# Kernel tuning notes

Measured on AMD Instinct MI355X. Metric: run time of the kernel, lower is better.

Reference implementation:

```python
import jax, jax.numpy as jnp
import numpy as np

N = 100000   # nodes
E = 1600000  # edges
NF = 8       # node features
H = 128      # hid_channel


def _gcn(x, ei, W, b):
    """PyG GCNConv: add self-loops, sym-normalize, x@W then scatter-add, +bias."""
    n = x.shape[0]
    loop = jnp.arange(n)
    s = jnp.concatenate([ei[0], loop])
    d = jnp.concatenate([ei[1], loop])
    deg = jax.ops.segment_sum(jnp.ones_like(s, jnp.float32), d, num_segments=n)
    dinv = jnp.where(deg > 0, jax.lax.rsqrt(deg), 0.0)
    norm = dinv[s] * dinv[d]                       # [E+n]
    xw = x @ W                                     # [n, out]
    out = jax.ops.segment_sum(xw[s] * norm[:, None], d, num_segments=n)
    return out + b


def _dag_pool(x, ei, k):
    """DAGPool(k): contiguous-k mean clustering; unpool restores saved (x, ei)."""
    n = x.shape[0]
    nc = -(-n // k)
    cid = jnp.arange(n) // k
    cnt = jax.ops.segment_sum(jnp.ones((n,), jnp.float32), cid, num_segments=nc)
    xp = jax.ops.segment_sum(x, cid, num_segments=nc) / cnt[:, None]
    return xp, ei // k, (x, ei)


def setup_inputs() -> dict:
    key = jax.random.key(0)
    ks = jax.random.split(key, 24)

    def w(k, i, o):
        return jax.random.normal(k, (i, o), jnp.float32) / np.sqrt(i).astype(np.float32)

    d = {
        "x": jax.random.normal(ks[0], (N, NF), jnp.float32),
        "edge_index": jax.random.randint(ks[1], (E, 2), 0, N, dtype=jnp.int64),
        "c1W": w(ks[2], NF, H),          "c1b": jnp.zeros((H,), jnp.float32),
        "c2W": w(ks[3], H + NF, H),      "c2b": jnp.zeros((H,), jnp.float32),
        "c3W": w(ks[4], H + NF, H),      "c3b": jnp.zeros((H,), jnp.float32),
        "c4W": w(ks[5], H, H),           "c4b": jnp.zeros((H,), jnp.float32),
        "c5W": w(ks[6], H, H),           "c5b": jnp.zeros((H,), jnp.float32),
        "f1W": w(ks[7], 2 * H + NF, H),  "f1b": jnp.zeros((H,), jnp.float32),
        "f2W": w(ks[8], 2 * H, H),       "f2b": jnp.zeros((H,), jnp.float32),
        "f3W": w(ks[9], 2 * H, H),       "f3b": jnp.zeros((H,), jnp.float32),
        "f4W": w(ks[10], H + NF, H),     "f4b": jnp.zeros((H,), jnp.float32),
        "f5W": w(ks[11], H + NF, 1),     "f5b": jnp.zeros((1,), jnp.float32),
    }
    return d


def reference(x, edge_index, c1W, c1b, c2W, c2b, c3W, c3b, c4W, c4b, c5W, c5b,
              f1W, f1b, f2W, f2b, f3W, f3b, f4W, f4b, f5W, f5b):
    ei = edge_index.T  # [2, E]
    x_in = x
    h = jax.nn.relu(_gcn(x, ei, c1W, c1b))
    h = jnp.concatenate([h, x_in], axis=-1)
    h = jax.nn.relu(_gcn(h, ei, c2W, c2b))
    h = jnp.concatenate([x_in, h], axis=-1)            # [N, NF+H]

    xp1, ei1, un1 = _dag_pool(h, ei, 5)
    t = jax.nn.relu(_gcn(xp1, ei1, c3W, c3b))
    t = jax.nn.relu(jnp.concatenate([xp1, t], -1) @ f1W + f1b)
    xp2, ei2, un2 = _dag_pool(t, ei1, 3)
    t = jax.nn.relu(_gcn(xp2, ei2, c4W, c4b))
    t = jax.nn.relu(jnp.concatenate([xp2, t], -1) @ f2W + f2b)
    xp3, ei3, un3 = _dag_pool(t, ei2, 3)
    t = jax.nn.relu(_gcn(xp3, ei3, c5W, c5b))
    t = jax.nn.relu(jnp.concatenate([xp3, t], -1) @ f3W + f3b)
    # unpool chain discards pooled features and restores pre-pool1 state
    xr, _ = un1

    h = jax.nn.relu(xr @ f4W + f4b)
    out = jax.nn.sigmoid(jnp.concatenate([x_in, h], -1) @ f5W + f5b)
    return out.ravel()  # [N], binary (num_classes==2 -> 1 logit)
```

## Files before the change

kernel.cpp:

```cpp
#include <hip/hip_runtime.h>
#include <hip/hip_bf16.h>
#include <math.h>


#define NBUK 128

typedef __attribute__((ext_vector_type(8))) short short8;
typedef __attribute__((ext_vector_type(4))) float f32x4;

__device__ __forceinline__ unsigned short f32_to_bf16_rne(float f) {
    unsigned u = __float_as_uint(f);
    return (unsigned short)((u + 0x7fffu + ((u >> 16) & 1u)) >> 16);
}

__global__ __launch_bounds__(512) void bucket_kernel(
    const int* __restrict__ ei, int* __restrict__ bcnt_pad,
    int2* __restrict__ bucket, int E, int N, int cap) {
    constexpr int EPB = 8192;
    __shared__ int lcnt[NBUK];
    __shared__ int lcur[NBUK];
    int e0 = blockIdx.x * EPB;
    int e1 = min(e0 + EPB, E);
    if (threadIdx.x < NBUK) lcnt[threadIdx.x] = 0;
    __syncthreads();
    for (int e = e0 + threadIdx.x; e < e1; e += 512) {
        int2 v = ((const int2*)ei)[e];
        if ((unsigned)v.y < (unsigned)N) {
            int b = (int)(((unsigned long long)(unsigned)v.y * NBUK) / (unsigned)N);
            atomicAdd(&lcnt[b], 1);
        }
    }
    __syncthreads();
    if (threadIdx.x < NBUK)
        lcur[threadIdx.x] = atomicAdd(&bcnt_pad[threadIdx.x * 16], lcnt[threadIdx.x]);
    __syncthreads();
    for (int e = e0 + threadIdx.x; e < e1; e += 512) {
        int2 v = ((const int2*)ei)[e];
        if ((unsigned)v.y < (unsigned)N) {
            int b = (int)(((unsigned long long)(unsigned)v.y * NBUK) / (unsigned)N);
            int pos = atomicAdd(&lcur[b], 1);
            if (pos < cap) {
                int s = ((unsigned)v.x < (unsigned)N) ? v.x : 0;
                bucket[(size_t)b * cap + pos] = make_int2(s, v.y);
            }
        }
    }
}

__global__ __launch_bounds__(1024) void csr_kernel(
    const int2* __restrict__ bucket, const int* __restrict__ bcnt_pad,
    int* __restrict__ cnt, int* __restrict__ rowstart, int* __restrict__ col,
    int N, int cap) {
    __shared__ int lcnt[1024];
    __shared__ int lscan[1024];
    int b = blockIdx.x;
    int lo = (int)(((long long)b * N + NBUK - 1) / NBUK);
    int hi = (int)(((long long)(b + 1) * N + NBUK - 1) / NBUK);
    int range = hi - lo;
    lcnt[threadIdx.x] = 0;
    __syncthreads();
    int n = min(bcnt_pad[b * 16], cap);
    const int2* bk = bucket + (size_t)b * cap;
    for (int i = threadIdx.x; i < n; i += 1024)
        atomicAdd(&lcnt[bk[i].y - lo], 1);
    __syncthreads();
    int myc = lcnt[threadIdx.x];
    if ((int)threadIdx.x < range) cnt[lo + threadIdx.x] = myc;
    lscan[threadIdx.x] = myc;
    __syncthreads();
    for (int off = 1; off < 1024; off <<= 1) {
        int y = (threadIdx.x >= off) ? lscan[threadIdx.x - off] : 0;
        __syncthreads();
        lscan[threadIdx.x] += y;
        __syncthreads();
    }
    int colbase = b * cap;
    int excl = lscan[threadIdx.x] - myc;
    if ((int)threadIdx.x < range) rowstart[lo + threadIdx.x] = colbase + excl;
    lcnt[threadIdx.x] = excl;
    __syncthreads();
    for (int i = threadIdx.x; i < n; i += 1024) {
        int2 v = bk[i];
        int pos = atomicAdd(&lcnt[v.y - lo], 1);
        col[(size_t)colbase + pos] = v.x;
    }
}

__global__ __launch_bounds__(256) void dinv_xs_kernel(const int* __restrict__ cnt,
                                                      const float* __restrict__ x,
                                                      float* __restrict__ dinv,
                                                      float* __restrict__ xs,
                                                      unsigned short* __restrict__ Abf2,
                                                      int n) {
    int v = blockIdx.x * 256 + threadIdx.x;
    if (v >= n) return;
    float dv = rsqrtf((float)(cnt[v] + 1));
    dinv[v] = dv;
    const float4* x4 = (const float4*)x;
    float4 a = x4[v * 2], b = x4[v * 2 + 1];
    float4* o = (float4*)xs;
    o[v * 2]     = make_float4(a.x * dv, a.y * dv, a.z * dv, a.w * dv);
    o[v * 2 + 1] = make_float4(b.x * dv, b.y * dv, b.z * dv, b.w * dv);
    unsigned short u[8] = {f32_to_bf16_rne(a.x), f32_to_bf16_rne(a.y),
                           f32_to_bf16_rne(a.z), f32_to_bf16_rne(a.w),
                           f32_to_bf16_rne(b.x), f32_to_bf16_rne(b.y),
                           f32_to_bf16_rne(b.z), f32_to_bf16_rne(b.w)};
    ulonglong2 pk;
    pk.x = (unsigned long long)u[0] | ((unsigned long long)u[1] << 16)
         | ((unsigned long long)u[2] << 32) | ((unsigned long long)u[3] << 48);
    pk.y = (unsigned long long)u[4] | ((unsigned long long)u[5] << 16)
         | ((unsigned long long)u[6] << 32) | ((unsigned long long)u[7] << 48);
    *(ulonglong2*)&Abf2[(size_t)v * 160] = pk;
    ulonglong2 z; z.x = 0ull; z.y = 0ull;
    *(ulonglong2*)&Abf2[(size_t)v * 160 + 136] = z;
    *(ulonglong2*)&Abf2[(size_t)v * 160 + 144] = z;
    *(ulonglong2*)&Abf2[(size_t)v * 160 + 152] = z;
}

__global__ __launch_bounds__(256) void agg8_kernel(const float* __restrict__ xs,
                                                   const int* __restrict__ rowstart,
                                                   const int* __restrict__ cnt,
                                                   const int* __restrict__ col,
                                                   const float* __restrict__ dinv,
                                                   float* __restrict__ aggx,
                                                   unsigned short* __restrict__ Abf,
                                                   int n) {
    int v = blockIdx.x * 256 + threadIdx.x;
    if (v >= n) return;
    const float4* r4 = (const float4*)xs;
    float4 a = make_float4(0, 0, 0, 0), b = make_float4(0, 0, 0, 0);
    int start = rowstart[v];
    int end = start + cnt[v];
    for (int j = start; j < end; j++) {
        int s = col[j];
        float4 p = r4[(size_t)s * 2], q = r4[(size_t)s * 2 + 1];
        a.x += p.x; a.y += p.y; a.z += p.z; a.w += p.w;
        b.x += q.x; b.y += q.y; b.z += q.z; b.w += q.w;
    }
    float4 p = r4[(size_t)v * 2], q = r4[(size_t)v * 2 + 1];
    a.x += p.x; a.y += p.y; a.z += p.z; a.w += p.w;
    b.x += q.x; b.y += q.y; b.z += q.z; b.w += q.w;
    float dv = dinv[v];
    a = make_float4(a.x * dv, a.y * dv, a.z * dv, a.w * dv);
    b = make_float4(b.x * dv, b.y * dv, b.z * dv, b.w * dv);
    float4* o = (float4*)aggx;
    o[(size_t)v * 2]     = a;
    o[(size_t)v * 2 + 1] = b;
    unsigned short u[8] = {f32_to_bf16_rne(a.x), f32_to_bf16_rne(a.y),
                           f32_to_bf16_rne(a.z), f32_to_bf16_rne(a.w),
                           f32_to_bf16_rne(b.x), f32_to_bf16_rne(b.y),
                           f32_to_bf16_rne(b.z), f32_to_bf16_rne(b.w)};
    ulonglong2 pk;
    pk.x = (unsigned long long)u[0] | ((unsigned long long)u[1] << 16)
         | ((unsigned long long)u[2] << 32) | ((unsigned long long)u[3] << 48);
    pk.y = (unsigned long long)u[4] | ((unsigned long long)u[5] << 16)
         | ((unsigned long long)u[6] << 32) | ((unsigned long long)u[7] << 48);
    *(ulonglong2*)&Abf[(size_t)v * 160 + 128] = pk;
    ulonglong2 z; z.x = 0ull; z.y = 0ull;
    *(ulonglong2*)&Abf[(size_t)v * 160 + 136] = z;
    *(ulonglong2*)&Abf[(size_t)v * 160 + 144] = z;
    *(ulonglong2*)&Abf[(size_t)v * 160 + 152] = z;
}

__global__ __launch_bounds__(256) void agg128_kernel(const unsigned* __restrict__ rows,
                                                     const int* __restrict__ rowstart,
                                                     const int* __restrict__ cnt,
                                                     const int* __restrict__ col,
                                                     const float* __restrict__ dinv,
                                                     unsigned short* __restrict__ Abf,
                                                     int n) {
    int v = blockIdx.x * 4 + (threadIdx.x >> 6);
    int lane = threadIdx.x & 63;
    if (v >= n) return;
    float ax = 0.f, ay = 0.f;
    int start = rowstart[v];
    int end = start + cnt[v];
    for (int base = start; base < end; base += 64) {
        int m = end - base; if (m > 64) m = 64;
        int si = (lane < m) ? col[base + lane] : 0;
        int t = 0;
        for (; t + 4 <= m; t += 4) {
            int s0 = __shfl(si, t),     s1 = __shfl(si, t + 1);
            int s2 = __shfl(si, t + 2), s3 = __shfl(si, t + 3);
            unsigned u0 = rows[(size_t)s0 * 64 + lane];
            unsigned u1 = rows[(size_t)s1 * 64 + lane];
            unsigned u2 = rows[(size_t)s2 * 64 + lane];
            unsigned u3 = rows[(size_t)s3 * 64 + lane];
            ax += (__uint_as_float(u0 << 16) + __uint_as_float(u1 << 16))
                + (__uint_as_float(u2 << 16) + __uint_as_float(u3 << 16));
            ay += (__uint_as_float(u0 & 0xffff0000u) + __uint_as_float(u1 & 0xffff0000u))
                + (__uint_as_float(u2 & 0xffff0000u) + __uint_as_float(u3 & 0xffff0000u));
        }
        for (; t < m; t++) {
            int s = __shfl(si, t);
            unsigned u = rows[(size_t)s * 64 + lane];
            ax += __uint_as_float(u << 16);
            ay += __uint_as_float(u & 0xffff0000u);
        }
    }
    unsigned us = rows[(size_t)v * 64 + lane];
    ax += __uint_as_float(us << 16);
    ay += __uint_as_float(us & 0xffff0000u);
    float dv = dinv[v];
    unsigned pk = (unsigned)f32_to_bf16_rne(ax * dv)
                | ((unsigned)f32_to_bf16_rne(ay * dv) << 16);
    ((unsigned*)Abf)[(size_t)v * 80 + lane] = pk;
}

__global__ __launch_bounds__(256) void gemm8_kernel(
    const float* __restrict__ A1, const float* __restrict__ W,
    const float* __restrict__ bias, const float* __restrict__ dinv,
    unsigned short* __restrict__ out, int n) {
    constexpr int K = 8, KP = 12, NPB = 32;
    __shared__ float lds[NPB * KP];
    int node0 = blockIdx.x * NPB;
    for (int idx = threadIdx.x; idx < NPB * K; idx += 256) {
        int r = idx / K, k = idx - r * K;
        int node = node0 + r;
        lds[r * KP + k] = (node < n) ? A1[(size_t)node * K + k] : 0.f;
    }
    __syncthreads();
    int f8 = threadIdx.x & 15, ng = threadIdx.x >> 4;
    int fbase = f8 * 8;
    float acc[2][8];
#pragma unroll
    for (int r = 0; r < 2; r++)
#pragma unroll
        for (int j = 0; j < 8; j++) acc[r][j] = 0.f;
    for (int k = 0; k < K; k += 4) {
        float4 wlo[4], whi[4];
#pragma unroll
        for (int kk = 0; kk < 4; kk++) {
            wlo[kk] = *(const float4*)&W[(size_t)(k + kk) * 128 + fbase];
            whi[kk] = *(const float4*)&W[(size_t)(k + kk) * 128 + fbase + 4];
        }
#pragma unroll
        for (int r = 0; r < 2; r++) {
            float4 a = *(const float4*)&lds[(2 * ng + r) * KP + k];
            float av[4] = {a.x, a.y, a.z, a.w};
#pragma unroll
            for (int kk = 0; kk < 4; kk++) {
                acc[r][0] += av[kk] * wlo[kk].x; acc[r][1] += av[kk] * wlo[kk].y;
                acc[r][2] += av[kk] * wlo[kk].z; acc[r][3] += av[kk] * wlo[kk].w;
                acc[r][4] += av[kk] * whi[kk].x; acc[r][5] += av[kk] * whi[kk].y;
                acc[r][6] += av[kk] * whi[kk].z; acc[r][7] += av[kk] * whi[kk].w;
            }
        }
    }
    float4 blo = *(const float4*)&bias[fbase];
    float4 bhi = *(const float4*)&bias[fbase + 4];
    float bv[8] = {blo.x, blo.y, blo.z, blo.w, bhi.x, bhi.y, bhi.z, bhi.w};
#pragma unroll
    for (int r = 0; r < 2; r++) {
        int node = node0 + 2 * ng + r;
        if (node < n) {
            float dv = dinv[node];
            unsigned short u[8];
#pragma unroll
            for (int j = 0; j < 8; j++)
                u[j] = f32_to_bf16_rne(fmaxf(acc[r][j] + bv[j], 0.f) * dv);
            ulonglong2 pk;
            pk.x = (unsigned long long)u[0] | ((unsigned long long)u[1] << 16)
                 | ((unsigned long long)u[2] << 32) | ((unsigned long long)u[3] << 48);
            pk.y = (unsigned long long)u[4] | ((unsigned long long)u[5] << 16)
                 | ((unsigned long long)u[6] << 32) | ((unsigned long long)u[7] << 48);
            *(ulonglong2*)&out[(size_t)node * 128 + fbase] = pk;
        }
    }
}

__global__ __launch_bounds__(256) void pack_w_kernel(const float* __restrict__ W,
                                                     unsigned short* __restrict__ wp, int K) {
    int t = blockIdx.x * 256 + threadIdx.x;
    if (t >= 20480) return;
    int i = t & 7, l = (t >> 3) & 63, fc = (t >> 9) & 7, ks = t >> 12;
    int k = ks * 32 + (l >> 4) * 8 + i;
    int c = (l & 15) + 16 * fc;
    float v = (k < K) ? W[(size_t)k * 128 + c] : 0.f;
    wp[t] = f32_to_bf16_rne(v);
}

template <int MODE>
__global__ __launch_bounds__(256) void mfma_gemm(
    const unsigned short* __restrict__ A, const unsigned short* __restrict__ wp,
    const float* __restrict__ bias, const float* __restrict__ x,
    const float* __restrict__ f5W, const float* __restrict__ f5b,
    void* __restrict__ outv, int n) {
    __shared__ float ldsx[64];
    int node0 = blockIdx.x * 64;
    if constexpr (MODE == 2) {
        if (threadIdx.x < 64) {
            int rc = min(node0 + (int)threadIdx.x, n - 1);
            float s = 0.f;
#pragma unroll
            for (int k = 0; k < 8; k++) s += x[(size_t)rc * 8 + k] * f5W[k];
            ldsx[threadIdx.x] = s;
        }
        __syncthreads();
    }
    int wave = threadIdx.x >> 6, lane = threadIdx.x & 63;
    int g = lane >> 4, r = lane & 15;
    int row0 = node0 + wave * 16;
    int arow = min(row0 + r, n - 1);

    short8 a[5];
#pragma unroll
    for (int ks = 0; ks < 5; ks++)
        a[ks] = *(const short8*)&A[(size_t)arow * 160 + ks * 32 + g * 8];

    f32x4 acc[8] = {};
#pragma unroll
    for (int ks = 0; ks < 5; ks++) {
#pragma unroll
        for (int fc = 0; fc < 8; fc++) {
            short8 w = *(const short8*)&wp[(size_t)((ks * 8 + fc) * 64 + lane) * 8];
            acc[fc] = __builtin_amdgcn_mfma_f32_16x16x32_bf16(a[ks], w, acc[fc], 0, 0, 0);
        }
    }

    if constexpr (MODE == 1) {
        unsigned short* out = (unsigned short*)outv;
#pragma unroll
        for (int fc = 0; fc < 8; fc++) {
            int c = r + 16 * fc;
            float bc = bias[c];
#pragma unroll
            for (int v = 0; v < 4; v++) {
                int row = row0 + 4 * g + v;
                if (row < n)
                    out[(size_t)row * 160 + 8 + c] =
                        f32_to_bf16_rne(fmaxf(acc[fc][v] + bc, 0.f));
            }
        }
    } else {
        float plog[4] = {0.f, 0.f, 0.f, 0.f};
#pragma unroll
        for (int fc = 0; fc < 8; fc++) {
            int c = r + 16 * fc;
            float bc = bias[c];
            float w5 = f5W[8 + c];
#pragma unroll
            for (int v = 0; v < 4; v++)
                plog[v] += fmaxf(acc[fc][v] + bc, 0.f) * w5;
        }
#pragma unroll
        for (int m = 1; m < 16; m <<= 1) {
#pragma unroll
            for (int v = 0; v < 4; v++) plog[v] += __shfl_xor(plog[v], m);
        }
        if (r == 0) {
            float* out = (float*)outv;
            float fb = f5b[0];
#pragma unroll
            for (int v = 0; v < 4; v++) {
                int row = row0 + 4 * g + v;
                if (row < n)
                    out[row] = 1.f / (1.f + expf(-(plog[v] + ldsx[wave * 16 + 4 * g + v] + fb)));
            }
        }
    }
}

extern "C" void kernel_launch(void* const* d_in, const int* in_sizes, int n_in,
                              void* d_out, int out_size, void* d_ws, size_t ws_size,
                              hipStream_t stream) {
    const float* x   = (const float*)d_in[0];
    const int*   ei  = (const int*)d_in[1];
    const float* c1W = (const float*)d_in[2];
    const float* c1b = (const float*)d_in[3];
    const float* c2W = (const float*)d_in[4];
    const float* c2b = (const float*)d_in[5];
    const float* f4W = (const float*)d_in[18];
    const float* f4b = (const float*)d_in[19];
    const float* f5W = (const float*)d_in[20];
    const float* f5b = (const float*)d_in[21];
    float* out = (float*)d_out;

    int N = in_sizes[0] / 8;
    int E = in_sizes[1] / 2;

    char* p = (char*)d_ws;
    auto alloc = [&](size_t bytes) {
        char* q = p;
        p += (bytes + 255) & ~(size_t)255;
        return q;
    };
    const int cap = 14000;
    int*            cnt      = (int*)alloc((size_t)N * 4);
    int*            rowstart = (int*)alloc((size_t)N * 4);
    int*            bcnt_pad = (int*)alloc(NBUK * 16 * 4);
    float*          dinv     = (float*)alloc((size_t)N * 4);
    int*            col      = (int*)alloc((size_t)NBUK * cap * 4);
    float*          xs       = (float*)alloc((size_t)N * 8 * 4);
    float*          aggx     = (float*)alloc((size_t)N * 8 * 4);
    unsigned short* bufH1    = (unsigned short*)alloc((size_t)N * 128 * 2);
    unsigned short* Abf      = (unsigned short*)alloc((size_t)N * 160 * 2);
    unsigned short* Abf2     = (unsigned short*)alloc((size_t)N * 160 * 2);
    unsigned short* wp2      = (unsigned short*)alloc(20480 * 2);
    unsigned short* wp4      = (unsigned short*)alloc(20480 * 2);

    int2* bucket = (int2*)bufH1;

    (void)hipMemsetAsync(bcnt_pad, 0, NBUK * 16 * 4, stream);

    int gN = (N + 255) / 256;
    pack_w_kernel<<<80, 256, 0, stream>>>(c2W, wp2, 136);
    pack_w_kernel<<<80, 256, 0, stream>>>(f4W, wp4, 136);

    int gB = (E + 8191) / 8192;
    bucket_kernel<<<gB, 512, 0, stream>>>(ei, bcnt_pad, bucket, E, N, cap);

    csr_kernel<<<NBUK, 1024, 0, stream>>>(bucket, bcnt_pad, cnt, rowstart, col, N, cap);

    dinv_xs_kernel<<<gN, 256, 0, stream>>>(cnt, x, dinv, xs, Abf2, N);

    agg8_kernel<<<gN, 256, 0, stream>>>(xs, rowstart, cnt, col, dinv, aggx, Abf, N);

    gemm8_kernel<<<(N + 31) / 32, 256, 0, stream>>>(aggx, c1W, c1b, dinv, bufH1, N);

    agg128_kernel<<<(N + 3) / 4, 256, 0, stream>>>((const unsigned*)bufH1, rowstart,
                                                   cnt, col, dinv, Abf, N);

    int g64 = (N + 63) / 64;
    mfma_gemm<1><<<g64, 256, 0, stream>>>(Abf, wp2, c2b, nullptr, nullptr, nullptr,
                                          Abf2, N);
    mfma_gemm<2><<<g64, 256, 0, stream>>>(Abf2, wp4, f4b, x, f5W, f5b, out, N);
}
```

Before: 205.3 us.

## Split 128-wide aggregation into 8 feature slices for per-XCD L2 locality

The hidden-feature buffer is stored as 8 feature-slice planes of 16 bf16 per node instead of one 128-wide row per node, and gemm8 writes into this sliced layout. The 128-wide neighbour aggregation now runs as 8 slice passes, with the slice chosen by blockIdx&7 and 8 lanes per node. Under round-robin block dispatch each XCD should then gather from a single ~3.2MB plane that can stay in its L2, rather than from the whole 25.6MB buffer. The cost is 32-byte gathers in place of full 256-byte coalesced rows, more degree divergence with 8 nodes per wave, and int4 loads of col that assume 16-byte aligned row starts.

Result: slower. 236.7 us (+15.3%).

```diff
diff --git a/kernel.cpp b/kernel.cpp
--- a/kernel.cpp
+++ b/kernel.cpp
@@ -162,49 +162,46 @@
     *(ulonglong2*)&Abf[(size_t)v * 160 + 152] = z;
 }
 
-__global__ __launch_bounds__(256) void agg128_kernel(const unsigned* __restrict__ rows,
-                                                     const int* __restrict__ rowstart,
-                                                     const int* __restrict__ cnt,
-                                                     const int* __restrict__ col,
-                                                     const float* __restrict__ dinv,
-                                                     unsigned short* __restrict__ Abf,
-                                                     int n) {
-    int v = blockIdx.x * 4 + (threadIdx.x >> 6);
-    int lane = threadIdx.x & 63;
+__global__ __launch_bounds__(256) void agg128s_kernel(
+    const unsigned* __restrict__ rows,
+    const int* __restrict__ rowstart, const int* __restrict__ cnt,
+    const int* __restrict__ col, const float* __restrict__ dinv,
+    unsigned short* __restrict__ Abf, int n) {
+    int slice = blockIdx.x & 7;
+    int chunk = blockIdx.x >> 3;
+    int g  = threadIdx.x >> 3;
+    int fl = threadIdx.x & 7;
+    int v = chunk * 32 + g;
     if (v >= n) return;
+    const unsigned* base = rows + (size_t)slice * n * 8;
     float ax = 0.f, ay = 0.f;
     int start = rowstart[v];
-    int end = start + cnt[v];
-    for (int base = start; base < end; base += 64) {
-        int m = end - base; if (m > 64) m = 64;
-        int si = (lane < m) ? col[base + lane] : 0;
-        int t = 0;
-        for (; t + 4 <= m; t += 4) {
-            int s0 = __shfl(si, t),     s1 = __shfl(si, t + 1);
-            int s2 = __shfl(si, t + 2), s3 = __shfl(si, t + 3);
-            unsigned u0 = rows[(size_t)s0 * 64 + lane];
-            unsigned u1 = rows[(size_t)s1 * 64 + lane];
-            unsigned u2 = rows[(size_t)s2 * 64 + lane];
-            unsigned u3 = rows[(size_t)s3 * 64 + lane];
-            ax += (__uint_as_float(u0 << 16) + __uint_as_float(u1 << 16))
-                + (__uint_as_float(u2 << 16) + __uint_as_float(u3 << 16));
-            ay += (__uint_as_float(u0 & 0xffff0000u) + __uint_as_float(u1 & 0xffff0000u))
-                + (__uint_as_float(u2 & 0xffff0000u) + __uint_as_float(u3 & 0xffff0000u));
-        }
-        for (; t < m; t++) {
-            int s = __shfl(si, t);
-            unsigned u = rows[(size_t)s * 64 + lane];
-            ax += __uint_as_float(u << 16);
-            ay += __uint_as_float(u & 0xffff0000u);
-        }
-    }
-    unsigned us = rows[(size_t)v * 64 + lane];
+    int m = cnt[v];
+    int j = 0;
+    for (; j + 4 <= m; j += 4) {
+        int4 s4 = *(const int4*)&col[start + j];
+        unsigned u0 = base[(size_t)s4.x * 8 + fl];
+        unsigned u1 = base[(size_t)s4.y * 8 + fl];
+        unsigned u2 = base[(size_t)s4.z * 8 + fl];
+        unsigned u3 = base[(size_t)s4.w * 8 + fl];
+        ax += (__uint_as_float(u0 << 16) + __uint_as_float(u1 << 16))
+            + (__uint_as_float(u2 << 16) + __uint_as_float(u3 << 16));
+        ay += (__uint_as_float(u0 & 0xffff0000u) + __uint_as_float(u1 & 0xffff0000u))
+            + (__uint_as_float(u2 & 0xffff0000u) + __uint_as_float(u3 & 0xffff0000u));
+    }
+    for (; j < m; j++) {
+        int s = col[start + j];
+        unsigned u = base[(size_t)s * 8 + fl];
+        ax += __uint_as_float(u << 16);
+        ay += __uint_as_float(u & 0xffff0000u);
+    }
+    unsigned us = base[(size_t)v * 8 + fl];
     ax += __uint_as_float(us << 16);
     ay += __uint_as_float(us & 0xffff0000u);
     float dv = dinv[v];
     unsigned pk = (unsigned)f32_to_bf16_rne(ax * dv)
                 | ((unsigned)f32_to_bf16_rne(ay * dv) << 16);
-    ((unsigned*)Abf)[(size_t)v * 80 + lane] = pk;
+    ((unsigned*)Abf)[(size_t)v * 80 + slice * 8 + fl] = pk;
 }
 
 __global__ __launch_bounds__(256) void gemm8_kernel(
@@ -264,7 +261,8 @@
                  | ((unsigned long long)u[2] << 32) | ((unsigned long long)u[3] << 48);
             pk.y = (unsigned long long)u[4] | ((unsigned long long)u[5] << 16)
                  | ((unsigned long long)u[6] << 32) | ((unsigned long long)u[7] << 48);
-            *(ulonglong2*)&out[(size_t)node * 128 + fbase] = pk;
+            size_t off = ((size_t)(f8 >> 1) * n + node) * 16 + (size_t)(f8 & 1) * 8;
+            *(ulonglong2*)&out[off] = pk;
         }
     }
 }
@@ -418,8 +416,8 @@
 
     gemm8_kernel<<<(N + 31) / 32, 256, 0, stream>>>(aggx, c1W, c1b, dinv, bufH1, N);
 
-    agg128_kernel<<<(N + 3) / 4, 256, 0, stream>>>((const unsigned*)bufH1, rowstart,
-                                                   cnt, col, dinv, Abf, N);
+    agg128s_kernel<<<8 * ((N + 31) / 32), 256, 0, stream>>>(
+        (const unsigned*)bufH1, rowstart, cnt, col, dinv, Abf, N);
 
     int g64 = (N + 63) / 64;
     mfma_gemm<1><<<g64, 256, 0, stream>>>(Abf, wp2, c2b, nullptr, nullptr, nullptr,
```
